# Kernel optimization log

Hardware: AMD Instinct MI355X
Metric: run time of the kernel (lower is better)

## Reference

```python
import jax, jax.numpy as jnp
import numpy as np

EPS_ATTN = 1e-6
LN_EPS = 1e-5

def _layernorm(x, g, b):
    mu = jnp.mean(x, axis=-1, keepdims=True)
    var = jnp.var(x, axis=-1, keepdims=True)
    return (x - mu) * jax.lax.rsqrt(var + LN_EPS) * g + b

def _phi(x):
    return jax.nn.elu(x) + 1.0

def setup_inputs() -> dict:
    key = jax.random.key(0)
    ks = jax.random.split(key, 8)
    B, T, D, H = 2, 4096, 128, 128  # D = token_dim = d+1, H = hidden_dim
    s = 0.02
    return {
        "tokens": jax.random.normal(ks[0], (B, T, D), dtype=jnp.float32),
        "Wq": jax.random.normal(ks[1], (D, H), dtype=jnp.float32) * s,
        "Wk": jax.random.normal(ks[2], (D, H), dtype=jnp.float32) * s,
        "Wv": jax.random.normal(ks[3], (D, D), dtype=jnp.float32) * s,
        "Wg": jax.random.normal(ks[4], (D, D), dtype=jnp.float32) * s,
        "bg": jnp.zeros((D,), dtype=jnp.float32),
        "Wo": jax.random.normal(ks[5], (D, D), dtype=jnp.float32) * s,
        "g1": jnp.ones((D,), dtype=jnp.float32),
        "b1": jnp.zeros((D,), dtype=jnp.float32),
        "g2": jnp.ones((D,), dtype=jnp.float32),
        "b2": jnp.zeros((D,), dtype=jnp.float32),
    }

def reference(tokens, Wq, Wk, Wv, Wg, bg, Wo, g1, b1, g2, b2):
    x = _layernorm(tokens, g1, b1)                 # (b,t,m)
    Q = x @ Wq                                     # (b,t,h)
    K = x @ Wk                                     # (b,t,h)
    V = x @ Wv                                     # (b,t,m)
    G = jax.nn.sigmoid(x @ Wg + bg)                # (b,t,m)
    Vg = V * G
    Qp = _phi(Q)
    Kp = _phi(K)
    # causal linear attention via cumulative outer products
    kv = jnp.einsum('bth,btm->bthm', Kp, Vg)       # (b,t,h,m)
    S_kv = jnp.cumsum(kv, axis=1)
    S_k = jnp.cumsum(Kp, axis=1)
    numerator = jnp.einsum('bth,bthm->btm', Qp, S_kv)
    denom = jnp.maximum(jnp.einsum('bth,bth->bt', Qp, S_k), EPS_ATTN)
    attn_out = numerator / denom[..., None]
    out = tokens + (attn_out @ Wo) * 0.1
    return _layernorm(out, g2, b2)
```

## Files before the change

kernel.cpp:

```cpp
#include <hip/hip_runtime.h>
#include <math.h>

#define T_ 4096
#define D_ 128
#define NTOK 8192
#define CHUNK 64
#define NCB 64
#define NCH 128
#define LN_EPS 1e-5f
#define EPS_ATTN 1e-6f

typedef __attribute__((ext_vector_type(8))) short bf16x8;
typedef __attribute__((ext_vector_type(4))) short bf16x4;
typedef __attribute__((ext_vector_type(2))) short bf16x2;
typedef __attribute__((ext_vector_type(4))) float f32x4;

__device__ inline short f2bf(float f) {
  unsigned u = __builtin_bit_cast(unsigned, f);
  u += 0x7fffu + ((u >> 16) & 1u);
  return (short)(u >> 16);
}
__device__ inline float bf2f(short s) {
  unsigned u = ((unsigned)(unsigned short)s) << 16;
  return __builtin_bit_cast(float, u);
}
__device__ inline float phi_(float x) { return x > 0.f ? x + 1.f : __expf(x); }

__global__ __launch_bounds__(256) void k_wprep(const float* __restrict__ Wq,
    const float* __restrict__ Wk, const float* __restrict__ Wv,
    const float* __restrict__ Wg, const float* __restrict__ Wo,
    short* __restrict__ WT) {
  const float* W = blockIdx.x==0?Wq: blockIdx.x==1?Wk: blockIdx.x==2?Wv: blockIdx.x==3?Wg:Wo;
  short* out = WT + blockIdx.x*D_*D_;
  __shared__ float lds[128][132];
  const int tid = threadIdx.x;
  #pragma unroll
  for (int it = 0; it < 16; ++it) {
    const int f = it*1024 + tid*4;
    const int k = f >> 7, n = f & 127;
    const float4 v = *(const float4*)&W[f];
    lds[k][n] = v.x; lds[k][n+1] = v.y; lds[k][n+2] = v.z; lds[k][n+3] = v.w;
  }
  __syncthreads();
  #pragma unroll
  for (int it = 0; it < 16; ++it) {
    const int f = it*1024 + tid*4;
    const int n = f >> 7, k = f & 127;
    bf16x4 o;
    o.x = f2bf(lds[k][n]);   o.y = f2bf(lds[k+1][n]);
    o.z = f2bf(lds[k+2][n]); o.w = f2bf(lds[k+3][n]);
    *(bf16x4*)&out[f] = o;
  }
}

__global__ __launch_bounds__(256) void k_qkvg(const float* __restrict__ tokens,
    const short* __restrict__ WT,
    const float* __restrict__ g1, const float* __restrict__ b1,
    const float* __restrict__ bg,
    short* __restrict__ Qp, short* __restrict__ Kp, short* __restrict__ KpT,
    short* __restrict__ VgT) {
  const int m0 = blockIdx.x * 32;
  const int y = blockIdx.y;
  const int tid = threadIdx.x;
  const int w = tid >> 6, l = tid & 63;
  __shared__ short xs[32][136];
  __shared__ short wsd[128][136];

  {
    const float2 gg = *(const float2*)&g1[l*2];
    const float2 bb = *(const float2*)&b1[l*2];
    float2 tv[8];
    #pragma unroll
    for (int it = 0; it < 8; ++it)
      tv[it] = *(const float2*)&tokens[(m0 + w*8 + it)*D_ + l*2];
    #pragma unroll
    for (int it = 0; it < 8; ++it) {
      const float2 v = tv[it];
      float s = v.x + v.y, qq = v.x*v.x + v.y*v.y;
      #pragma unroll
      for (int off = 1; off < 64; off <<= 1) {
        s += __shfl_xor(s, off); qq += __shfl_xor(qq, off);
      }
      const float mean = s*(1.f/D_);
      const float r2 = rsqrtf(qq*(1.f/D_) - mean*mean + LN_EPS);
      bf16x2 o;
      o.x = f2bf((v.x-mean)*r2*gg.x + bb.x);
      o.y = f2bf((v.y-mean)*r2*gg.y + bb.y);
      *(bf16x2*)&xs[w*8 + it][l*2] = o;
    }
  }

  auto stageW = [&](const short* __restrict__ Wb) {
    for (int v = tid; v < 2048; v += 256) {
      const int n = v >> 4, c8 = (v & 15)*8;
      *(bf16x8*)&wsd[n][c8] = *(const bf16x8*)&Wb[n*D_ + c8];
    }
  };

  const int i = l & 15, q = l >> 4;
  auto gemm = [&](f32x4 (*acc)[2]) {
    #pragma unroll
    for (int kk = 0; kk < 4; ++kk) {
      bf16x8 a[2], bfr[2];
      #pragma unroll
      for (int mt = 0; mt < 2; ++mt) a[mt] = *(const bf16x8*)&xs[mt*16+i][kk*32+q*8];
      #pragma unroll
      for (int nt = 0; nt < 2; ++nt) bfr[nt] = *(const bf16x8*)&wsd[w*32+nt*16+i][kk*32+q*8];
      #pragma unroll
      for (int mt = 0; mt < 2; ++mt)
        #pragma unroll
        for (int nt = 0; nt < 2; ++nt)
          acc[mt][nt] = __builtin_amdgcn_mfma_f32_16x16x32_bf16(a[mt], bfr[nt], acc[mt][nt], 0, 0, 0);
    }
  };

  stageW(WT + (y == 2 ? 2 : y)*D_*D_);
  __syncthreads();
  f32x4 acc[2][2];
  #pragma unroll
  for (int mt = 0; mt < 2; ++mt)
    #pragma unroll
    for (int nt = 0; nt < 2; ++nt) acc[mt][nt] = (f32x4){0.f,0.f,0.f,0.f};
  gemm(acc);

  if (y == 0) {
    #pragma unroll
    for (int mt = 0; mt < 2; ++mt)
      #pragma unroll
      for (int nt = 0; nt < 2; ++nt) {
        const int h = w*32 + nt*16 + i;
        #pragma unroll
        for (int r = 0; r < 4; ++r)
          Qp[(m0 + mt*16 + 4*q + r)*D_ + h] = f2bf(phi_(acc[mt][nt][r]));
      }
  } else if (y == 1) {
    #pragma unroll
    for (int mt = 0; mt < 2; ++mt)
      #pragma unroll
      for (int nt = 0; nt < 2; ++nt) {
        const int h = w*32 + nt*16 + i;
        const int t0 = m0 + mt*16 + 4*q;
        bf16x4 o;
        #pragma unroll
        for (int r = 0; r < 4; ++r) {
          const short bv = f2bf(phi_(acc[mt][nt][r]));
          Kp[(t0+r)*D_ + h] = bv;
          o[r] = bv;
        }
        *(bf16x4*)&KpT[h*NTOK + t0] = o;
      }
  } else {
    __syncthreads();
    stageW(WT + 3*D_*D_);
    __syncthreads();
    f32x4 accg[2][2];
    #pragma unroll
    for (int mt = 0; mt < 2; ++mt)
      #pragma unroll
      for (int nt = 0; nt < 2; ++nt) accg[mt][nt] = (f32x4){0.f,0.f,0.f,0.f};
    gemm(accg);
    #pragma unroll
    for (int mt = 0; mt < 2; ++mt)
      #pragma unroll
      for (int nt = 0; nt < 2; ++nt) {
        const int h = w*32 + nt*16 + i;
        const int t0 = m0 + mt*16 + 4*q;
        const float bgd = bg[h];
        bf16x4 o;
        #pragma unroll
        for (int r = 0; r < 4; ++r) {
          const float gv = 1.f/(1.f + __expf(-(accg[mt][nt][r] + bgd)));
          o[r] = f2bf(acc[mt][nt][r] * gv);
        }
        *(bf16x4*)&VgT[h*NTOK + t0] = o;
      }
  }
}

__global__ __launch_bounds__(256) void k_chunkkv(const short* __restrict__ KpT,
    const short* __restrict__ VgT,
    float* __restrict__ KVT, float* __restrict__ Ksum) {
  const int c = blockIdx.x, hh = blockIdx.y, dh = blockIdx.z;
  const int tid = threadIdx.x;
  const int tb = c*CHUNK;
  __shared__ short vgl[64][72];
  __shared__ short kpl[64][72];
  __shared__ float ksp[64][5];
  for (int u = tid; u < 512; u += 256) {
    const int dd = u >> 3, c8 = (u & 7)*8;
    *(bf16x8*)&vgl[dd][c8] = *(const bf16x8*)&VgT[(dh*64+dd)*NTOK + tb + c8];
    *(bf16x8*)&kpl[dd][c8] = *(const bf16x8*)&KpT[(hh*64+dd)*NTOK + tb + c8];
  }
  __syncthreads();
  const int w = tid >> 6, l = tid & 63, i = l & 15, q = l >> 4;
  f32x4 acc[4];
  #pragma unroll
  for (int nt = 0; nt < 4; ++nt) acc[nt] = (f32x4){0.f,0.f,0.f,0.f};
  #pragma unroll
  for (int kk = 0; kk < 2; ++kk) {
    bf16x8 a = *(const bf16x8*)&vgl[w*16+i][kk*32+q*8];
    #pragma unroll
    for (int nt = 0; nt < 4; ++nt) {
      bf16x8 bb = *(const bf16x8*)&kpl[nt*16+i][kk*32+q*8];
      acc[nt] = __builtin_amdgcn_mfma_f32_16x16x32_bf16(a, bb, acc[nt], 0, 0, 0);
    }
  }
  float* KVc = KVT + (size_t)c*16384;
  #pragma unroll
  for (int nt = 0; nt < 4; ++nt)
    #pragma unroll
    for (int r = 0; r < 4; ++r) {
      const int d = dh*64 + w*16 + 4*q + r;
      const int h = hh*64 + nt*16 + i;
      KVc[d*D_ + h] = acc[nt][r];
    }
  if (dh == 0) {
    const int h = tid >> 2, part = tid & 3;
    float s = 0.f;
    #pragma unroll
    for (int t = 0; t < 16; ++t) s += bf2f(kpl[h][part*16 + t]);
    ksp[h][part] = s;
    __syncthreads();
    if (tid < 64)
      Ksum[c*D_ + hh*64 + tid] = ksp[tid][0]+ksp[tid][1]+ksp[tid][2]+ksp[tid][3];
  }
}

__global__ __launch_bounds__(256) void k_prescore(const float* __restrict__ KVT,
    short* __restrict__ KVTb, float* __restrict__ Ksum,
    const short* __restrict__ Qp, const short* __restrict__ Kp,
    short* __restrict__ A, float* __restrict__ rowsum) {
  const int tid = threadIdx.x;
  if (blockIdx.x < 128) {
    const int b = blockIdx.x >> 6;
    const int e = (blockIdx.x & 63)*256 + tid;
    const size_t base = (size_t)b*NCB*16384 + e;
    float run = 0.f;
    #pragma unroll 8
    for (int c = 0; c < NCB; ++c) {
      const float v = KVT[base + (size_t)c*16384];
      KVTb[base + (size_t)c*16384] = f2bf(run);
      run += v;
    }
    return;
  }
  if (blockIdx.x == 128) {
    const int b = tid >> 7, h = tid & 127;
    float run = 0.f;
    #pragma unroll 8
    for (int c = 0; c < NCB; ++c) {
      const int idx = (b*NCB + c)*128 + h;
      const float v = Ksum[idx];
      Ksum[idx] = run;
      run += v;
    }
    return;
  }
  const int c = blockIdx.x - 129;
  const int tb = c*CHUNK;
  __shared__ short qpl[64][136], kpl[64][136];
  #pragma unroll
  for (int u = tid; u < 1024; u += 256) {
    const int t = u >> 4, c8 = (u & 15)*8;
    *(bf16x8*)&qpl[t][c8] = *(const bf16x8*)&Qp[(tb+t)*D_ + c8];
    *(bf16x8*)&kpl[t][c8] = *(const bf16x8*)&Kp[(tb+t)*D_ + c8];
  }
  __syncthreads();
  const int w = tid >> 6, l = tid & 63, i = l & 15, q = l >> 4;
  f32x4 acc[4];
  #pragma unroll
  for (int nt = 0; nt < 4; ++nt) acc[nt] = (f32x4){0.f,0.f,0.f,0.f};
  #pragma unroll
  for (int kk = 0; kk < 4; ++kk) {
    bf16x8 a = *(const bf16x8*)&qpl[w*16+i][kk*32+q*8];
    for (int nt = 0; nt <= w; ++nt) {
      bf16x8 bb = *(const bf16x8*)&kpl[nt*16+i][kk*32+q*8];
      acc[nt] = __builtin_amdgcn_mfma_f32_16x16x32_bf16(a, bb, acc[nt], 0, 0, 0);
    }
  }
  short* Ac = A + c*4096;
  float rs[4] = {0.f,0.f,0.f,0.f};
  #pragma unroll
  for (int nt = 0; nt < 4; ++nt) {
    #pragma unroll
    for (int r = 0; r < 4; ++r) {
      const int t = w*16 + 4*q + r;
      const int s = nt*16 + i;
      const float v = (nt <= w && s <= t) ? acc[nt][r] : 0.f;
      rs[r] += v;
      Ac[t*64 + s] = f2bf(v);
    }
  }
  #pragma unroll
  for (int r = 0; r < 4; ++r) {
    #pragma unroll
    for (int off = 1; off < 16; off <<= 1) rs[r] += __shfl_xor(rs[r], off);
  }
  if (i == 0) {
    #pragma unroll
    for (int r = 0; r < 4; ++r) rowsum[c*64 + w*16 + 4*q + r] = rs[r];
  }
}

__global__ __launch_bounds__(256) void k_attnout(const short* __restrict__ Aintra,
    const short* __restrict__ Qp, const short* __restrict__ VgT,
    const short* __restrict__ KVTb, const float* __restrict__ Ksum,
    const float* __restrict__ rowsum, short* __restrict__ attn) {
  const int c = blockIdx.x, dq = blockIdx.y, tid = threadIdx.x;
  const int tb = c*CHUNK;
  __shared__ short at[64][200], bt[32][200];
  __shared__ float ksl[128], dpart[64][4], denl[64];
  const short* Ac = Aintra + c*4096;
  #pragma unroll
  for (int u = tid; u < 512; u += 256) {
    const int t = u >> 3, c8 = (u & 7)*8;
    *(bf16x8*)&at[t][c8] = *(const bf16x8*)&Ac[t*64 + c8];
  }
  #pragma unroll
  for (int u = tid; u < 1024; u += 256) {
    const int t = u >> 4, c8 = (u & 15)*8;
    *(bf16x8*)&at[t][64 + c8] = *(const bf16x8*)&Qp[(tb+t)*D_ + c8];
  }
  for (int u = tid; u < 256; u += 256) {
    const int dd = u >> 3, c8 = (u & 7)*8;
    *(bf16x8*)&bt[dd][c8] = *(const bf16x8*)&VgT[(dq*32+dd)*NTOK + tb + c8];
  }
  #pragma unroll
  for (int u = tid; u < 512; u += 256) {
    const int dd = u >> 4, c8 = (u & 15)*8;
    *(bf16x8*)&bt[dd][64 + c8] = *(const bf16x8*)&KVTb[(size_t)c*16384 + (dq*32+dd)*D_ + c8];
  }
  if (tid < 128) ksl[tid] = Ksum[c*128 + tid];
  __syncthreads();
  {
    const int t = tid >> 2, part = tid & 3;
    float dot = 0.f;
    #pragma unroll
    for (int h = 0; h < 32; ++h) dot += bf2f(at[t][64 + part*32 + h]) * ksl[part*32 + h];
    dpart[t][part] = dot;
  }
  __syncthreads();
  if (tid < 64)
    denl[tid] = fmaxf(rowsum[c*64 + tid] + dpart[tid][0]+dpart[tid][1]+dpart[tid][2]+dpart[tid][3], EPS_ATTN);
  __syncthreads();
  const int w = tid >> 6, l = tid & 63, i = l & 15, q = l >> 4;
  f32x4 acc[2];
  #pragma unroll
  for (int nt = 0; nt < 2; ++nt) acc[nt] = (f32x4){0.f,0.f,0.f,0.f};
  #pragma unroll
  for (int kk = 0; kk < 6; ++kk) {
    bf16x8 a = *(const bf16x8*)&at[w*16+i][kk*32+q*8];
    #pragma unroll
    for (int nt = 0; nt < 2; ++nt) {
      bf16x8 bb = *(const bf16x8*)&bt[nt*16+i][kk*32+q*8];
      acc[nt] = __builtin_amdgcn_mfma_f32_16x16x32_bf16(a, bb, acc[nt], 0, 0, 0);
    }
  }
  #pragma unroll
  for (int r = 0; r < 4; ++r) {
    const int t = w*16 + 4*q + r;
    const float inv = 1.f / denl[t];
    #pragma unroll
    for (int nt = 0; nt < 2; ++nt)
      attn[(size_t)(tb+t)*D_ + dq*32 + nt*16 + i] = f2bf(acc[nt][r] * inv);
  }
}

__global__ __launch_bounds__(256) void k_outln2(const short* __restrict__ attn,
    const short* __restrict__ WoT, const float* __restrict__ tokens,
    const float* __restrict__ g2, const float* __restrict__ b2,
    float* __restrict__ out) {
  const int m0 = blockIdx.x*16, tid = threadIdx.x;
  __shared__ short al[16][136], wl[128][136];
  __shared__ float tl[16][132];
  __shared__ float suml[16][4], ssql[16][4];
  __shared__ float meanl[16], rstdl[16];
  __shared__ float gl[128], bl2[128];
  for (int u = tid; u < 256; u += 256) {
    const int t = u >> 4, c8 = (u & 15)*8;
    *(bf16x8*)&al[t][c8] = *(const bf16x8*)&attn[(m0+t)*D_ + c8];
  }
  #pragma unroll
  for (int u = tid; u < 2048; u += 256) {
    const int n = u >> 4, c8 = (u & 15)*8;
    *(bf16x8*)&wl[n][c8] = *(const bf16x8*)&WoT[n*D_ + c8];
  }
  #pragma unroll
  for (int u = tid; u < 512; u += 256) {
    const int t = u >> 5, c4 = (u & 31)*4;
    *(float4*)&tl[t][c4] = *(const float4*)&tokens[(m0+t)*D_ + c4];
  }
  if (tid < 128) { gl[tid] = g2[tid]; bl2[tid] = b2[tid]; }
  __syncthreads();
  const int w = tid >> 6, l = tid & 63, i = l & 15, q = l >> 4;
  f32x4 acc[2];
  #pragma unroll
  for (int j = 0; j < 2; ++j) acc[j] = (f32x4){0.f,0.f,0.f,0.f};
  #pragma unroll
  for (int kk = 0; kk < 4; ++kk) {
    bf16x8 a = *(const bf16x8*)&al[i][kk*32+q*8];
    #pragma unroll
    for (int j = 0; j < 2; ++j) {
      bf16x8 bb = *(const bf16x8*)&wl[(w*2+j)*16+i][kk*32+q*8];
      acc[j] = __builtin_amdgcn_mfma_f32_16x16x32_bf16(a, bb, acc[j], 0, 0, 0);
    }
  }
  float p[4][2], ps[4], qs[4];
  #pragma unroll
  for (int r = 0; r < 4; ++r) {
    const int t = 4*q + r;
    ps[r] = 0.f; qs[r] = 0.f;
    #pragma unroll
    for (int j = 0; j < 2; ++j) {
      const int col = w*32 + j*16 + i;
      const float v = tl[t][col] + 0.1f*acc[j][r];
      p[r][j] = v; ps[r] += v; qs[r] += v*v;
    }
  }
  #pragma unroll
  for (int r = 0; r < 4; ++r) {
    #pragma unroll
    for (int off = 1; off < 16; off <<= 1) {
      ps[r] += __shfl_xor(ps[r], off);
      qs[r] += __shfl_xor(qs[r], off);
    }
  }
  if (i == 0) {
    #pragma unroll
    for (int r = 0; r < 4; ++r) {
      suml[4*q+r][w] = ps[r];
      ssql[4*q+r][w] = qs[r];
    }
  }
  __syncthreads();
  if (tid < 16) {
    const float s = suml[tid][0]+suml[tid][1]+suml[tid][2]+suml[tid][3];
    const float qq = ssql[tid][0]+ssql[tid][1]+ssql[tid][2]+ssql[tid][3];
    const float mean = s*(1.f/D_);
    meanl[tid] = mean;
    rstdl[tid] = rsqrtf(qq*(1.f/D_) - mean*mean + LN_EPS);
  }
  __syncthreads();
  #pragma unroll
  for (int r = 0; r < 4; ++r) {
    const int t = 4*q + r;
    const float mean = meanl[t], rr = rstdl[t];
    #pragma unroll
    for (int j = 0; j < 2; ++j) {
      const int col = w*32 + j*16 + i;
      out[(m0+t)*D_ + col] = (p[r][j]-mean)*rr*gl[col] + bl2[col];
    }
  }
}

extern "C" void kernel_launch(void* const* d_in, const int* in_sizes, int n_in,
                              void* d_out, int out_size, void* d_ws, size_t ws_size,
                              hipStream_t stream) {
  const float* tokens = (const float*)d_in[0];
  const float* Wq = (const float*)d_in[1];
  const float* Wk = (const float*)d_in[2];
  const float* Wv = (const float*)d_in[3];
  const float* Wg = (const float*)d_in[4];
  const float* bg = (const float*)d_in[5];
  const float* Wo = (const float*)d_in[6];
  const float* g1 = (const float*)d_in[7];
  const float* b1 = (const float*)d_in[8];
  const float* g2 = (const float*)d_in[9];
  const float* b2 = (const float*)d_in[10];

  char* base = (char*)d_ws;
  short* Qp     = (short*)(base);
  short* Kp     = (short*)(base + (2u<<20));
  short* KpT    = (short*)(base + (4u<<20));
  short* VgT    = (short*)(base + (6u<<20));
  short* attn   = (short*)(base + (8u<<20));
  short* KVTb   = (short*)(base + (10u<<20));
  short* Aintra = (short*)(base + (14u<<20));
  short* WT     = (short*)(base + (15u<<20));
  float* rowsum = (float*)(base + (15u<<20) + (256u<<10));
  float* Ksum   = (float*)(base + (15u<<20) + (512u<<10));
  float* KVT    = (float*)(base + (16u<<20));

  short* WoT = WT + 4*D_*D_;

  k_wprep<<<5, 256, 0, stream>>>(Wq, Wk, Wv, Wg, Wo, WT);
  k_qkvg<<<dim3(NTOK/32, 3), 256, 0, stream>>>(tokens, WT, g1, b1, bg,
                                               Qp, Kp, KpT, VgT);
  k_chunkkv<<<dim3(NCH, 2, 2), 256, 0, stream>>>(KpT, VgT, KVT, Ksum);
  k_prescore<<<257, 256, 0, stream>>>(KVT, KVTb, Ksum, Qp, Kp, Aintra, rowsum);
  k_attnout<<<dim3(NCH, 4), 256, 0, stream>>>(Aintra, Qp, VgT, KVTb, Ksum, rowsum, attn);
  k_outln2<<<NTOK/16, 256, 0, stream>>>(attn, WoT, tokens, g2, b2, (float*)d_out);
}
```

Measured before the change: 114.2 us.

## Fuse intra-chunk scores into attnout, move LN1 into weight-prep kernel

Layernorm-1 moves out of k_qkvg into the weight-prep kernel, which writes a bf16 normalized activation buffer once instead of recomputing it in all three qkvg column groups. The intra-chunk causal QK^T score computation moves from k_prescore into k_attnout, so the score matrix and row sums stay in LDS and are never round-tripped through global memory. k_attnout now covers 64 output columns per block over a 128x2 grid instead of 128x4. The cost is one extra global write and read of the normalized activations, fewer and heavier attnout blocks, and a redundant score recomputation in each of the two column blocks.

New measurement: 116.3 us. About the same (+1.8%).

```diff
diff --git a/kernel.cpp b/kernel.cpp
--- a/kernel.cpp
+++ b/kernel.cpp
@@ -26,37 +26,63 @@
 }
 __device__ inline float phi_(float x) { return x > 0.f ? x + 1.f : __expf(x); }
 
-__global__ __launch_bounds__(256) void k_wprep(const float* __restrict__ Wq,
+__global__ __launch_bounds__(256) void k_prep(const float* __restrict__ Wq,
     const float* __restrict__ Wk, const float* __restrict__ Wv,
     const float* __restrict__ Wg, const float* __restrict__ Wo,
-    short* __restrict__ WT) {
-  const float* W = blockIdx.x==0?Wq: blockIdx.x==1?Wk: blockIdx.x==2?Wv: blockIdx.x==3?Wg:Wo;
-  short* out = WT + blockIdx.x*D_*D_;
-  __shared__ float lds[128][132];
+    const float* __restrict__ tokens, const float* __restrict__ g1,
+    const float* __restrict__ b1,
+    short* __restrict__ WT, short* __restrict__ xb) {
   const int tid = threadIdx.x;
-  #pragma unroll
-  for (int it = 0; it < 16; ++it) {
-    const int f = it*1024 + tid*4;
-    const int k = f >> 7, n = f & 127;
-    const float4 v = *(const float4*)&W[f];
-    lds[k][n] = v.x; lds[k][n+1] = v.y; lds[k][n+2] = v.z; lds[k][n+3] = v.w;
-  }
-  __syncthreads();
-  #pragma unroll
-  for (int it = 0; it < 16; ++it) {
-    const int f = it*1024 + tid*4;
-    const int n = f >> 7, k = f & 127;
-    bf16x4 o;
-    o.x = f2bf(lds[k][n]);   o.y = f2bf(lds[k+1][n]);
-    o.z = f2bf(lds[k+2][n]); o.w = f2bf(lds[k+3][n]);
-    *(bf16x4*)&out[f] = o;
-  }
-}
-
-__global__ __launch_bounds__(256) void k_qkvg(const float* __restrict__ tokens,
-    const short* __restrict__ WT,
-    const float* __restrict__ g1, const float* __restrict__ b1,
-    const float* __restrict__ bg,
+  if (blockIdx.x < 5) {
+    const float* W = blockIdx.x==0?Wq: blockIdx.x==1?Wk: blockIdx.x==2?Wv: blockIdx.x==3?Wg:Wo;
+    short* out = WT + blockIdx.x*D_*D_;
+    __shared__ float lds[128][132];
+    #pragma unroll
+    for (int it = 0; it < 16; ++it) {
+      const int f = it*1024 + tid*4;
+      const int k = f >> 7, n = f & 127;
+      const float4 v = *(const float4*)&W[f];
+      lds[k][n] = v.x; lds[k][n+1] = v.y; lds[k][n+2] = v.z; lds[k][n+3] = v.w;
+    }
+    __syncthreads();
+    #pragma unroll
+    for (int it = 0; it < 16; ++it) {
+      const int f = it*1024 + tid*4;
+      const int n = f >> 7, k = f & 127;
+      bf16x4 o;
+      o.x = f2bf(lds[k][n]);   o.y = f2bf(lds[k+1][n]);
+      o.z = f2bf(lds[k+2][n]); o.w = f2bf(lds[k+3][n]);
+      *(bf16x4*)&out[f] = o;
+    }
+  } else {
+    const int m0 = (blockIdx.x - 5) * 32;
+    const int w = tid >> 6, l = tid & 63;
+    const float2 gg = *(const float2*)&g1[l*2];
+    const float2 bb = *(const float2*)&b1[l*2];
+    float2 tv[8];
+    #pragma unroll
+    for (int it = 0; it < 8; ++it)
+      tv[it] = *(const float2*)&tokens[(m0 + w*8 + it)*D_ + l*2];
+    #pragma unroll
+    for (int it = 0; it < 8; ++it) {
+      const float2 v = tv[it];
+      float s = v.x + v.y, qq = v.x*v.x + v.y*v.y;
+      #pragma unroll
+      for (int off = 1; off < 64; off <<= 1) {
+        s += __shfl_xor(s, off); qq += __shfl_xor(qq, off);
+      }
+      const float mean = s*(1.f/D_);
+      const float r2 = rsqrtf(qq*(1.f/D_) - mean*mean + LN_EPS);
+      bf16x2 o;
+      o.x = f2bf((v.x-mean)*r2*gg.x + bb.x);
+      o.y = f2bf((v.y-mean)*r2*gg.y + bb.y);
+      *(bf16x2*)&xb[(m0 + w*8 + it)*D_ + l*2] = o;
+    }
+  }
+}
+
+__global__ __launch_bounds__(256) void k_qkvg(const short* __restrict__ xb,
+    const short* __restrict__ WT, const float* __restrict__ bg,
     short* __restrict__ Qp, short* __restrict__ Kp, short* __restrict__ KpT,
     short* __restrict__ VgT) {
   const int m0 = blockIdx.x * 32;
@@ -66,28 +92,9 @@
   __shared__ short xs[32][136];
   __shared__ short wsd[128][136];
 
-  {
-    const float2 gg = *(const float2*)&g1[l*2];
-    const float2 bb = *(const float2*)&b1[l*2];
-    float2 tv[8];
-    #pragma unroll
-    for (int it = 0; it < 8; ++it)
-      tv[it] = *(const float2*)&tokens[(m0 + w*8 + it)*D_ + l*2];
-    #pragma unroll
-    for (int it = 0; it < 8; ++it) {
-      const float2 v = tv[it];
-      float s = v.x + v.y, qq = v.x*v.x + v.y*v.y;
-      #pragma unroll
-      for (int off = 1; off < 64; off <<= 1) {
-        s += __shfl_xor(s, off); qq += __shfl_xor(qq, off);
-      }
-      const float mean = s*(1.f/D_);
-      const float r2 = rsqrtf(qq*(1.f/D_) - mean*mean + LN_EPS);
-      bf16x2 o;
-      o.x = f2bf((v.x-mean)*r2*gg.x + bb.x);
-      o.y = f2bf((v.y-mean)*r2*gg.y + bb.y);
-      *(bf16x2*)&xs[w*8 + it][l*2] = o;
-    }
+  for (int u = tid; u < 512; u += 256) {
+    const int t = u >> 4, c8 = (u & 15)*8;
+    *(bf16x8*)&xs[t][c8] = *(const bf16x8*)&xb[(m0+t)*D_ + c8];
   }
 
   auto stageW = [&](const short* __restrict__ Wb) {
@@ -226,10 +233,8 @@
   }
 }
 
-__global__ __launch_bounds__(256) void k_prescore(const float* __restrict__ KVT,
-    short* __restrict__ KVTb, float* __restrict__ Ksum,
-    const short* __restrict__ Qp, const short* __restrict__ Kp,
-    short* __restrict__ A, float* __restrict__ rowsum) {
+__global__ __launch_bounds__(256) void k_prefix(const float* __restrict__ KVT,
+    short* __restrict__ KVTb, float* __restrict__ Ksum) {
   const int tid = threadIdx.x;
   if (blockIdx.x < 128) {
     const int b = blockIdx.x >> 6;
@@ -242,9 +247,7 @@
       KVTb[base + (size_t)c*16384] = f2bf(run);
       run += v;
     }
-    return;
-  }
-  if (blockIdx.x == 128) {
+  } else {
     const int b = tid >> 7, h = tid & 127;
     float run = 0.f;
     #pragma unroll 8
@@ -254,106 +257,88 @@
       Ksum[idx] = run;
       run += v;
     }
-    return;
-  }
-  const int c = blockIdx.x - 129;
+  }
+}
+
+__global__ __launch_bounds__(256) void k_attnout(const short* __restrict__ Qp,
+    const short* __restrict__ Kp, const short* __restrict__ VgT,
+    const short* __restrict__ KVTb, const float* __restrict__ Ksum,
+    short* __restrict__ attn) {
+  const int c = blockIdx.x, dh = blockIdx.y, tid = threadIdx.x;
   const int tb = c*CHUNK;
-  __shared__ short qpl[64][136], kpl[64][136];
-  #pragma unroll
-  for (int u = tid; u < 1024; u += 256) {
-    const int t = u >> 4, c8 = (u & 15)*8;
-    *(bf16x8*)&qpl[t][c8] = *(const bf16x8*)&Qp[(tb+t)*D_ + c8];
-    *(bf16x8*)&kpl[t][c8] = *(const bf16x8*)&Kp[(tb+t)*D_ + c8];
-  }
-  __syncthreads();
+  __shared__ short at[64][200], bt[64][200];
+  __shared__ float ksl[128], rsl[64], dpart[64][4], denl[64];
   const int w = tid >> 6, l = tid & 63, i = l & 15, q = l >> 4;
-  f32x4 acc[4];
-  #pragma unroll
-  for (int nt = 0; nt < 4; ++nt) acc[nt] = (f32x4){0.f,0.f,0.f,0.f};
-  #pragma unroll
-  for (int kk = 0; kk < 4; ++kk) {
-    bf16x8 a = *(const bf16x8*)&qpl[w*16+i][kk*32+q*8];
-    for (int nt = 0; nt <= w; ++nt) {
-      bf16x8 bb = *(const bf16x8*)&kpl[nt*16+i][kk*32+q*8];
-      acc[nt] = __builtin_amdgcn_mfma_f32_16x16x32_bf16(a, bb, acc[nt], 0, 0, 0);
-    }
-  }
-  short* Ac = A + c*4096;
-  float rs[4] = {0.f,0.f,0.f,0.f};
-  #pragma unroll
-  for (int nt = 0; nt < 4; ++nt) {
+  for (int v = tid; v < 1024; v += 256) {
+    const int t = v >> 4, c8 = (v & 15)*8;
+    *(bf16x8*)&at[t][64 + c8] = *(const bf16x8*)&Qp[(tb+t)*D_ + c8];
+    *(bf16x8*)&bt[t][c8]      = *(const bf16x8*)&Kp[(tb+t)*D_ + c8];
+  }
+  if (tid < 128) ksl[tid] = Ksum[c*D_ + tid];
+  __syncthreads();
+  {
+    f32x4 acc[4];
+    #pragma unroll
+    for (int nt = 0; nt < 4; ++nt) acc[nt] = (f32x4){0.f,0.f,0.f,0.f};
+    #pragma unroll
+    for (int kk = 0; kk < 4; ++kk) {
+      bf16x8 a = *(const bf16x8*)&at[w*16+i][64 + kk*32+q*8];
+      for (int nt = 0; nt <= w; ++nt) {
+        bf16x8 bb = *(const bf16x8*)&bt[nt*16+i][kk*32+q*8];
+        acc[nt] = __builtin_amdgcn_mfma_f32_16x16x32_bf16(a, bb, acc[nt], 0, 0, 0);
+      }
+    }
+    float rs[4] = {0.f,0.f,0.f,0.f};
+    #pragma unroll
+    for (int nt = 0; nt < 4; ++nt)
+      #pragma unroll
+      for (int r = 0; r < 4; ++r) {
+        const int t = w*16 + 4*q + r;
+        const int s = nt*16 + i;
+        const float v = (nt <= w && s <= t) ? acc[nt][r] : 0.f;
+        rs[r] += v;
+        at[t][s] = f2bf(v);
+      }
     #pragma unroll
     for (int r = 0; r < 4; ++r) {
-      const int t = w*16 + 4*q + r;
-      const int s = nt*16 + i;
-      const float v = (nt <= w && s <= t) ? acc[nt][r] : 0.f;
-      rs[r] += v;
-      Ac[t*64 + s] = f2bf(v);
-    }
-  }
-  #pragma unroll
-  for (int r = 0; r < 4; ++r) {
-    #pragma unroll
-    for (int off = 1; off < 16; off <<= 1) rs[r] += __shfl_xor(rs[r], off);
-  }
-  if (i == 0) {
-    #pragma unroll
-    for (int r = 0; r < 4; ++r) rowsum[c*64 + w*16 + 4*q + r] = rs[r];
-  }
-}
-
-__global__ __launch_bounds__(256) void k_attnout(const short* __restrict__ Aintra,
-    const short* __restrict__ Qp, const short* __restrict__ VgT,
-    const short* __restrict__ KVTb, const float* __restrict__ Ksum,
-    const float* __restrict__ rowsum, short* __restrict__ attn) {
-  const int c = blockIdx.x, dq = blockIdx.y, tid = threadIdx.x;
-  const int tb = c*CHUNK;
-  __shared__ short at[64][200], bt[32][200];
-  __shared__ float ksl[128], dpart[64][4], denl[64];
-  const short* Ac = Aintra + c*4096;
-  #pragma unroll
-  for (int u = tid; u < 512; u += 256) {
-    const int t = u >> 3, c8 = (u & 7)*8;
-    *(bf16x8*)&at[t][c8] = *(const bf16x8*)&Ac[t*64 + c8];
-  }
-  #pragma unroll
-  for (int u = tid; u < 1024; u += 256) {
-    const int t = u >> 4, c8 = (u & 15)*8;
-    *(bf16x8*)&at[t][64 + c8] = *(const bf16x8*)&Qp[(tb+t)*D_ + c8];
-  }
-  for (int u = tid; u < 256; u += 256) {
-    const int dd = u >> 3, c8 = (u & 7)*8;
-    *(bf16x8*)&bt[dd][c8] = *(const bf16x8*)&VgT[(dq*32+dd)*NTOK + tb + c8];
-  }
-  #pragma unroll
-  for (int u = tid; u < 512; u += 256) {
-    const int dd = u >> 4, c8 = (u & 15)*8;
-    *(bf16x8*)&bt[dd][64 + c8] = *(const bf16x8*)&KVTb[(size_t)c*16384 + (dq*32+dd)*D_ + c8];
-  }
-  if (tid < 128) ksl[tid] = Ksum[c*128 + tid];
-  __syncthreads();
+      #pragma unroll
+      for (int off = 1; off < 16; off <<= 1) rs[r] += __shfl_xor(rs[r], off);
+    }
+    if (i == 0) {
+      #pragma unroll
+      for (int r = 0; r < 4; ++r) rsl[w*16 + 4*q + r] = rs[r];
+    }
+  }
   {
     const int t = tid >> 2, part = tid & 3;
     float dot = 0.f;
     #pragma unroll
-    for (int h = 0; h < 32; ++h) dot += bf2f(at[t][64 + part*32 + h]) * ksl[part*32 + h];
+    for (int h = 0; h < 32; ++h)
+      dot += bf2f(at[t][64 + part*32 + h]) * ksl[part*32 + h];
     dpart[t][part] = dot;
   }
   __syncthreads();
   if (tid < 64)
-    denl[tid] = fmaxf(rowsum[c*64 + tid] + dpart[tid][0]+dpart[tid][1]+dpart[tid][2]+dpart[tid][3], EPS_ATTN);
-  __syncthreads();
-  const int w = tid >> 6, l = tid & 63, i = l & 15, q = l >> 4;
-  f32x4 acc[2];
-  #pragma unroll
-  for (int nt = 0; nt < 2; ++nt) acc[nt] = (f32x4){0.f,0.f,0.f,0.f};
+    denl[tid] = fmaxf(rsl[tid] + dpart[tid][0]+dpart[tid][1]+dpart[tid][2]+dpart[tid][3], EPS_ATTN);
+  for (int v = tid; v < 512; v += 256) {
+    const int dd = v >> 3, c8 = (v & 7)*8;
+    *(bf16x8*)&bt[dd][c8] = *(const bf16x8*)&VgT[(dh*64+dd)*NTOK + tb + c8];
+  }
+  for (int v = tid; v < 1024; v += 256) {
+    const int dd = v >> 4, c8 = (v & 15)*8;
+    *(bf16x8*)&bt[dd][64 + c8] = *(const bf16x8*)&KVTb[(size_t)c*16384 + (dh*64+dd)*D_ + c8];
+  }
+  __syncthreads();
+  f32x4 acc2[4];
+  #pragma unroll
+  for (int nt = 0; nt < 4; ++nt) acc2[nt] = (f32x4){0.f,0.f,0.f,0.f};
   #pragma unroll
   for (int kk = 0; kk < 6; ++kk) {
     bf16x8 a = *(const bf16x8*)&at[w*16+i][kk*32+q*8];
     #pragma unroll
-    for (int nt = 0; nt < 2; ++nt) {
+    for (int nt = 0; nt < 4; ++nt) {
       bf16x8 bb = *(const bf16x8*)&bt[nt*16+i][kk*32+q*8];
-      acc[nt] = __builtin_amdgcn_mfma_f32_16x16x32_bf16(a, bb, acc[nt], 0, 0, 0);
+      acc2[nt] = __builtin_amdgcn_mfma_f32_16x16x32_bf16(a, bb, acc2[nt], 0, 0, 0);
     }
   }
   #pragma unroll
@@ -361,8 +346,8 @@
     const int t = w*16 + 4*q + r;
     const float inv = 1.f / denl[t];
     #pragma unroll
-    for (int nt = 0; nt < 2; ++nt)
-      attn[(size_t)(tb+t)*D_ + dq*32 + nt*16 + i] = f2bf(acc[nt][r] * inv);
+    for (int nt = 0; nt < 4; ++nt)
+      attn[(size_t)(tb+t)*D_ + dh*64 + nt*16 + i] = f2bf(acc2[nt][r] * inv);
   }
 }
 
@@ -469,25 +454,23 @@
   const float* b2 = (const float*)d_in[10];
 
   char* base = (char*)d_ws;
-  short* Qp     = (short*)(base);
-  short* Kp     = (short*)(base + (2u<<20));
-  short* KpT    = (short*)(base + (4u<<20));
-  short* VgT    = (short*)(base + (6u<<20));
-  short* attn   = (short*)(base + (8u<<20));
-  short* KVTb   = (short*)(base + (10u<<20));
-  short* Aintra = (short*)(base + (14u<<20));
-  short* WT     = (short*)(base + (15u<<20));
-  float* rowsum = (float*)(base + (15u<<20) + (256u<<10));
-  float* Ksum   = (float*)(base + (15u<<20) + (512u<<10));
+  short* xb     = (short*)(base);
+  short* Qp     = (short*)(base + (2u<<20));
+  short* Kp     = (short*)(base + (4u<<20));
+  short* KpT    = (short*)(base + (6u<<20));
+  short* VgT    = (short*)(base + (8u<<20));
+  short* attn   = (short*)(base + (10u<<20));
+  short* KVTb   = (short*)(base + (12u<<20));
   float* KVT    = (float*)(base + (16u<<20));
+  short* WT     = (short*)(base + (24u<<20));
+  float* Ksum   = (float*)(base + (24u<<20) + (256u<<10));
 
   short* WoT = WT + 4*D_*D_;
 
-  k_wprep<<<5, 256, 0, stream>>>(Wq, Wk, Wv, Wg, Wo, WT);
-  k_qkvg<<<dim3(NTOK/32, 3), 256, 0, stream>>>(tokens, WT, g1, b1, bg,
-                                               Qp, Kp, KpT, VgT);
+  k_prep<<<261, 256, 0, stream>>>(Wq, Wk, Wv, Wg, Wo, tokens, g1, b1, WT, xb);
+  k_qkvg<<<dim3(NTOK/32, 3), 256, 0, stream>>>(xb, WT, bg, Qp, Kp, KpT, VgT);
   k_chunkkv<<<dim3(NCH, 2, 2), 256, 0, stream>>>(KpT, VgT, KVT, Ksum);
-  k_prescore<<<257, 256, 0, stream>>>(KVT, KVTb, Ksum, Qp, Kp, Aintra, rowsum);
-  k_attnout<<<dim3(NCH, 4), 256, 0, stream>>>(Aintra, Qp, VgT, KVTb, Ksum, rowsum, attn);
+  k_prefix<<<129, 256, 0, stream>>>(KVT, KVTb, Ksum);
+  k_attnout<<<dim3(NCH, 2), 256, 0, stream>>>(Qp, Kp, VgT, KVTb, Ksum, attn);
   k_outln2<<<NTOK/16, 256, 0, stream>>>(attn, WoT, tokens, g2, b2, (float*)d_out);
 }
```
